# Optimization experiments

Hardware: AMD Instinct MI355X
Metric: run time of the kernel (lower is better)

## Reference

```python
import jax, jax.numpy as jnp
import numpy as np

D_MODEL = 1024
NUM_HEADS = 16
HEAD_SIZE = D_MODEL // NUM_HEADS
THETA = 10000.0
MAX_SEQ_LEN = 4096


def _rope_tables():
    # (max_seq_len, head_size//2) cos/sin tables, matching RotaryPositionalEmbedding
    k = jnp.arange(HEAD_SIZE // 2, dtype=jnp.float32)
    inv_freq = 1.0 / (THETA ** (2.0 * k / HEAD_SIZE))
    pos = jnp.arange(MAX_SEQ_LEN, dtype=jnp.float32)
    ang = pos[:, None] * inv_freq[None, :]
    return jnp.cos(ang), jnp.sin(ang)


def _apply_rope(x, cos, sin):
    # x: (b, h, s, d); cos/sin: (s, d//2) -> broadcast over (b, h)
    x1 = x[..., ::2]
    x2 = x[..., 1::2]
    out_even = x1 * cos - x2 * sin
    out_odd = x2 * cos + x1 * sin
    # re-interleave pairs back to (..., d)
    return jnp.stack([out_even, out_odd], axis=-1).reshape(x.shape)


def setup_inputs() -> dict:
    key = jax.random.key(0)
    k1, k2, k3 = jax.random.split(key, 3)
    b, s = 1, 4096
    std_qkv = np.sqrt(2.0 / (D_MODEL + 3 * D_MODEL))
    std_o = np.sqrt(2.0 / (D_MODEL + D_MODEL))
    return {
        "x": jax.random.normal(k1, (b, s, D_MODEL), dtype=jnp.float32),
        "token_positions": jnp.arange(s, dtype=jnp.int32),
        "W_qkv": jax.random.normal(k2, (3 * D_MODEL, D_MODEL), dtype=jnp.float32) * std_qkv,
        "W_o": jax.random.normal(k3, (D_MODEL, D_MODEL), dtype=jnp.float32) * std_o,
    }


def reference(x, token_positions, W_qkv, W_o):
    b, s, _ = x.shape
    qkv = jnp.einsum("bsd,ed->bse", x, W_qkv)  # (b, s, 3*d_model)
    q, k, v = jnp.split(qkv, 3, axis=-1)

    def to_heads(t):
        return t.reshape(b, s, NUM_HEADS, HEAD_SIZE).transpose(0, 2, 1, 3)  # (b, h, s, hs)

    q, k, v = to_heads(q), to_heads(k), to_heads(v)

    cos_tab, sin_tab = _rope_tables()
    cos = cos_tab[token_positions]  # (s, hs//2)
    sin = sin_tab[token_positions]
    q = _apply_rope(q, cos, sin)
    k = _apply_rope(k, cos, sin)

    scale = 1.0 / jnp.sqrt(jnp.asarray(HEAD_SIZE, dtype=x.dtype))
    scores = jnp.einsum("bhqd,bhkd->bhqk", q, k) * scale  # (b, h, s, s)
    causal = jnp.tril(jnp.ones((s, s), dtype=bool))
    scores = jnp.where(causal, scores, jnp.finfo(scores.dtype).min)
    attn = jax.nn.softmax(scores, axis=-1)
    out = jnp.einsum("bhqk,bhkd->bhqd", attn, v)  # (b, h, s, hs)
    out = out.transpose(0, 2, 1, 3).reshape(b, s, D_MODEL)
    return jnp.einsum("bsd,ed->bse", out, W_o)
```

## Files before the change

kernel.cpp:

```cpp
#include <hip/hip_runtime.h>
#include <stdint.h>

typedef unsigned short u16;
typedef __attribute__((ext_vector_type(8))) short bf16x8;
typedef __attribute__((ext_vector_type(4))) float f32x4;

#define LN_THETA 9.210340371976184f
#define SLEN 4096
#define DMODEL 1024

__device__ __forceinline__ u16 f2bf(float f) {
  union { float f; unsigned u; } v; v.f = f;
  unsigned u = v.u;
  return (u16)((u + 0x7FFFu + ((u >> 16) & 1u)) >> 16);
}
__device__ __forceinline__ u16 f2bf_trunc(float f) {
  union { float f; unsigned u; } v; v.f = f;
  return (u16)(v.u >> 16);
}

__device__ __forceinline__ f32x4 mfma16(bf16x8 a, bf16x8 b, f32x4 c) {
  return __builtin_amdgcn_mfma_f32_16x16x32_bf16(a, b, c, 0, 0, 0);
}

__device__ __forceinline__ void async16(const u16* g, u16* l) {
  __builtin_amdgcn_global_load_lds(
      (const __attribute__((address_space(1))) unsigned int*)g,
      (__attribute__((address_space(3))) unsigned int*)l, 16, 0, 0);
}

__global__ void rope_tab_kernel(const int* __restrict__ tokpos,
                                float2* __restrict__ tab) {
  int t = blockIdx.x * 256 + threadIdx.x;
  int s = t >> 5, i = t & 31;
  float inv = expf(-(float)(2 * i) * (LN_THETA / 64.0f));
  float ang = (float)tokpos[s] * inv;
  float sn, cs;
  sincosf(ang, &sn, &cs);
  tab[t] = make_float2(cs, sn);
}

__global__ void cvt_all_kernel(const float* __restrict__ x,
                               const float* __restrict__ wqkv,
                               const float* __restrict__ wo,
                               u16* __restrict__ xb, u16* __restrict__ wqkvb,
                               u16* __restrict__ wob) {
  int i = blockIdx.x * 256 + threadIdx.x;
  const float* src;
  u16* dst;
  if (i < (1 << 20)) {
    src = x; dst = xb;
  } else if (i < (1 << 20) + (3 << 18)) {
    i -= (1 << 20); src = wqkv; dst = wqkvb;
  } else {
    i -= (1 << 20) + (3 << 18); src = wo; dst = wob;
  }
  float4 v = ((const float4*)src)[i];
  ushort4 o;
  o.x = f2bf(v.x); o.y = f2bf(v.y); o.z = f2bf(v.z); o.w = f2bf(v.w);
  ((ushort4*)dst)[i] = o;
}

__global__ __launch_bounds__(256) void gemm_qkv_kernel(
    const u16* __restrict__ A, const u16* __restrict__ B,
    u16* __restrict__ qb, u16* __restrict__ kb,
    u16* __restrict__ vbT, const float2* __restrict__ cstab) {
  const int K = 1024;
  __shared__ __align__(16) u16 As[128][32];
  __shared__ __align__(16) u16 Bs[128][32];
  __shared__ __align__(16) u16 Ts[128][136];
  const int tid = threadIdx.x;
  const int wave = tid >> 6, lane = tid & 63;
  const int quad = lane >> 4, col = lane & 15;
  const int rowBase = blockIdx.x * 128;
  const int colBase = blockIdx.y * 128;
  const int wm = (wave >> 1) * 64, wn = (wave & 1) * 64;

  const int sRow = wave * 32 + (lane >> 2);
  const int sK = (lane & 3) * 8;
  const u16* gA = A + (size_t)(rowBase + sRow) * K + sK;
  const u16* gB = B + (size_t)(colBase + sRow) * K + sK;

  f32x4 acc[4][4];
#pragma unroll
  for (int i = 0; i < 4; ++i)
#pragma unroll
    for (int j = 0; j < 4; ++j)
      acc[i][j] = f32x4{0.f, 0.f, 0.f, 0.f};

  for (int kk = 0; kk < K; kk += 32) {
    __syncthreads();
    async16(gA + kk, &As[sRow][sK]);
    async16(gA + kk + 16 * K, &As[sRow + 16][sK]);
    async16(gB + kk, &Bs[sRow][sK]);
    async16(gB + kk + 16 * K, &Bs[sRow + 16][sK]);
    __syncthreads();
    bf16x8 af[4], bfr[4];
#pragma unroll
    for (int i = 0; i < 4; ++i)
      af[i] = *(const bf16x8*)&As[wm + i * 16 + col][quad * 8];
#pragma unroll
    for (int j = 0; j < 4; ++j)
      bfr[j] = *(const bf16x8*)&Bs[wn + j * 16 + col][quad * 8];
#pragma unroll
    for (int i = 0; i < 4; ++i)
#pragma unroll
      for (int j = 0; j < 4; ++j)
        acc[i][j] = mfma16(af[i], bfr[j], acc[i][j]);
  }

  const int sec = rowBase >> 10;

  if (sec < 2) {
#pragma unroll
    for (int j = 0; j < 4; ++j) {
      int sl = wn + j * 16 + col;
      int s = colBase + sl;
#pragma unroll
      for (int i = 0; i < 4; ++i) {
        int el = wm + i * 16 + quad * 4;
        int d = (rowBase + el) & 63;
        float v0 = acc[i][j][0], v1 = acc[i][j][1];
        float v2 = acc[i][j][2], v3 = acc[i][j][3];
        float2 cs0 = cstab[s * 32 + (d >> 1)];
        float2 cs1 = cstab[s * 32 + (d >> 1) + 1];
        ushort4 pk;
        pk.x = f2bf(v0 * cs0.x - v1 * cs0.y);
        pk.y = f2bf(v1 * cs0.x + v0 * cs0.y);
        pk.z = f2bf(v2 * cs1.x - v3 * cs1.y);
        pk.w = f2bf(v3 * cs1.x + v2 * cs1.y);
        *(ushort4*)&Ts[sl][el] = pk;
      }
    }
    __syncthreads();
    int sl = tid >> 1, hf = tid & 1;
    int hh = ((rowBase & 1023) >> 6) + hf;
    u16* dst = (sec == 0 ? qb : kb) + ((size_t)hh * SLEN + colBase + sl) * 64;
    const u16* srcp = &Ts[sl][hf * 64];
#pragma unroll
    for (int kq = 0; kq < 8; ++kq)
      ((int4*)dst)[kq] = ((const int4*)srcp)[kq];
  } else {
#pragma unroll
    for (int j = 0; j < 4; ++j) {
      int sl = wn + j * 16 + col;
#pragma unroll
      for (int i = 0; i < 4; ++i) {
        int el = wm + i * 16 + quad * 4;
#pragma unroll
        for (int r = 0; r < 4; ++r)
          Ts[el + r][sl] = f2bf(acc[i][j][r]);
      }
    }
    __syncthreads();
    int el = tid >> 1, sh = tid & 1;
    int e = rowBase - 2048 + el;
    int hh = e >> 6, d = e & 63;
    u16* dst = vbT + (size_t)(hh * 64 + d) * SLEN + colBase + sh * 64;
    const u16* srcp = &Ts[el][sh * 64];
#pragma unroll
    for (int kq = 0; kq < 8; ++kq)
      ((int4*)dst)[kq] = ((const int4*)srcp)[kq];
  }
}

__global__ __launch_bounds__(256) void gemm_out_kernel(
    const u16* __restrict__ A, const u16* __restrict__ B,
    float* __restrict__ outf) {
  const int K = 1024;
  __shared__ __align__(16) u16 As[128][32];
  __shared__ __align__(16) u16 Bs[64][32];
  const int tid = threadIdx.x;
  const int wave = tid >> 6, lane = tid & 63;
  const int quad = lane >> 4, col = lane & 15;
  const int rowBase = blockIdx.x * 128;
  const int colBase = blockIdx.y * 64;

  const int sRow = wave * 32 + (lane >> 2);
  const int bRow = wave * 16 + (lane >> 2);
  const int sK = (lane & 3) * 8;
  const u16* gA = A + (size_t)(rowBase + sRow) * K + sK;
  const u16* gB = B + (size_t)(colBase + bRow) * K + sK;

  f32x4 acc[2][4];
#pragma unroll
  for (int i = 0; i < 2; ++i)
#pragma unroll
    for (int j = 0; j < 4; ++j)
      acc[i][j] = f32x4{0.f, 0.f, 0.f, 0.f};

  for (int kk = 0; kk < K; kk += 32) {
    __syncthreads();
    async16(gA + kk, &As[sRow][sK]);
    async16(gA + kk + 16 * K, &As[sRow + 16][sK]);
    async16(gB + kk, &Bs[bRow][sK]);
    __syncthreads();
    bf16x8 af[2], bfr[4];
#pragma unroll
    for (int i = 0; i < 2; ++i)
      af[i] = *(const bf16x8*)&As[wave * 32 + i * 16 + col][quad * 8];
#pragma unroll
    for (int j = 0; j < 4; ++j)
      bfr[j] = *(const bf16x8*)&Bs[j * 16 + col][quad * 8];
#pragma unroll
    for (int i = 0; i < 2; ++i)
#pragma unroll
      for (int j = 0; j < 4; ++j)
        acc[i][j] = mfma16(af[i], bfr[j], acc[i][j]);
  }

#pragma unroll
  for (int i = 0; i < 2; ++i) {
    int r0 = rowBase + wave * 32 + i * 16 + quad * 4;
#pragma unroll
    for (int j = 0; j < 4; ++j) {
      int cc = colBase + j * 16 + col;
#pragma unroll
      for (int r = 0; r < 4; ++r)
        outf[(size_t)(r0 + r) * DMODEL + cc] = acc[i][j][r];
    }
  }
}

__global__ __launch_bounds__(128) void flash_kernel(
    const u16* __restrict__ qbuf, const u16* __restrict__ kbuf,
    const u16* __restrict__ vbT, u16* __restrict__ attn) {
  const int S = SLEN;
  const int h = blockIdx.x;
  const int tile = 63 - (int)blockIdx.y;
  const int wave = threadIdx.x >> 6, lane = threadIdx.x & 63;
  const int quad = lane >> 4, col = lane & 15;
  const u16* Q = qbuf + (size_t)h * S * 64;
  const u16* Kh = kbuf + (size_t)h * S * 64;
  const u16* Vt = vbT + (size_t)h * 64 * S;

  __shared__ __align__(16) u16 Ks[64][64];
  __shared__ __align__(16) u16 Vs[64][64];
  __shared__ __align__(16) u16 Pld[2][2][16][72];

  const int sr = lane >> 3;
  const int sw = ((lane & 7) ^ sr) * 8;
  const int dcol = (lane & 7) * 8;
  const int segA = ((quad ^ (col & 7)) * 8);
  const int segB = (((quad ^ 4) ^ (col & 7)) * 8);

  const int nch = tile + 1;
  const int qrow0 = tile * 64 + wave * 32;

  bf16x8 qf0[2], qf1[2];
#pragma unroll
  for (int i = 0; i < 2; ++i) {
    const u16* qp = &Q[(size_t)(qrow0 + i * 16 + col) * 64 + quad * 8];
    qf0[i] = *(const bf16x8*)qp;
    qf1[i] = *(const bf16x8*)(qp + 32);
  }

  f32x4 o[2][4];
#pragma unroll
  for (int i = 0; i < 2; ++i)
#pragma unroll
    for (int n = 0; n < 4; ++n) o[i][n] = f32x4{0.f, 0.f, 0.f, 0.f};
  float lrow[2][4] = {{0.f, 0.f, 0.f, 0.f}, {0.f, 0.f, 0.f, 0.f}};

  for (int c = 0; c < nch; ++c) {
    const int k0 = c * 64;
    __syncthreads();
    {
#pragma unroll
      for (int t = 0; t < 4; ++t) {
        int row = (t * 2 + wave) * 8 + sr;
        async16(Kh + (size_t)(k0 + row) * 64 + sw, &Ks[row][dcol]);
        async16(Vt + (size_t)row * S + k0 + sw, &Vs[row][dcol]);
      }
    }
    __syncthreads();

    bf16x8 kf0[4], kf1[4], vf0[4], vf1[4];
#pragma unroll
    for (int j = 0; j < 4; ++j) {
      kf0[j] = *(const bf16x8*)&Ks[16 * j + col][segA];
      kf1[j] = *(const bf16x8*)&Ks[16 * j + col][segB];
    }
#pragma unroll
    for (int n = 0; n < 4; ++n) {
      vf0[n] = *(const bf16x8*)&Vs[16 * n + col][segA];
      vf1[n] = *(const bf16x8*)&Vs[16 * n + col][segB];
    }
    const bool lastc = (c == nch - 1);
#pragma unroll
    for (int i = 0; i < 2; ++i) {
      f32x4 s[4];
#pragma unroll
      for (int j = 0; j < 4; ++j)
        s[j] = mfma16(qf1[i], kf1[j],
                      mfma16(qf0[i], kf0[j], f32x4{0.f, 0.f, 0.f, 0.f}));
      float p[4][4];
#pragma unroll
      for (int r = 0; r < 4; ++r) {
        const int qrel = wave * 32 + i * 16 + quad * 4 + r;
#pragma unroll
        for (int j = 0; j < 4; ++j) {
          float e = __expf(s[j][r] * 0.125f);
          if (lastc && (16 * j + col > qrel)) e = 0.f;
          p[j][r] = e;
        }
        lrow[i][r] += (p[0][r] + p[1][r]) + (p[2][r] + p[3][r]);
      }
#pragma unroll
      for (int j = 0; j < 4; ++j)
#pragma unroll
        for (int r = 0; r < 4; ++r)
          Pld[wave][i][quad * 4 + r][16 * j + col] = f2bf_trunc(p[j][r]);
      bf16x8 pa0 = *(const bf16x8*)&Pld[wave][i][col][quad * 8];
      bf16x8 pa1 = *(const bf16x8*)&Pld[wave][i][col][quad * 8 + 32];
#pragma unroll
      for (int n = 0; n < 4; ++n)
        o[i][n] = mfma16(pa1, vf1[n], mfma16(pa0, vf0[n], o[i][n]));
    }
  }

#pragma unroll
  for (int i = 0; i < 2; ++i) {
#pragma unroll
    for (int m = 1; m <= 8; m <<= 1)
#pragma unroll
      for (int r = 0; r < 4; ++r) lrow[i][r] += __shfl_xor(lrow[i][r], m);
#pragma unroll
    for (int r = 0; r < 4; ++r) {
      float inv = 1.0f / lrow[i][r];
      int row = qrow0 + i * 16 + quad * 4 + r;
      u16* dst = &attn[(size_t)row * DMODEL + h * 64 + col];
#pragma unroll
      for (int n = 0; n < 4; ++n) dst[16 * n] = f2bf(o[i][n][r] * inv);
    }
  }
}

extern "C" void kernel_launch(void* const* d_in, const int* in_sizes, int n_in,
                              void* d_out, int out_size, void* d_ws,
                              size_t ws_size, hipStream_t stream) {
  const float* x = (const float*)d_in[0];
  const int* tokpos = (const int*)d_in[1];
  const float* wqkv = (const float*)d_in[2];
  const float* wo = (const float*)d_in[3];
  float* out = (float*)d_out;

  char* ws = (char*)d_ws;
  u16* xb    = (u16*)(ws);
  u16* wqkvb = (u16*)(ws + ((size_t)8 << 20));
  u16* wob   = (u16*)(ws + ((size_t)14 << 20));
  u16* qb    = (u16*)(ws + ((size_t)16 << 20));
  u16* kb    = (u16*)(ws + ((size_t)24 << 20));
  u16* vbT   = (u16*)(ws + ((size_t)32 << 20));
  u16* attn  = (u16*)(ws + ((size_t)40 << 20));
  float2* cstab = (float2*)(ws + ((size_t)48 << 20));

  rope_tab_kernel<<<dim3(512), dim3(256), 0, stream>>>(tokpos, cstab);
  cvt_all_kernel<<<dim3(8192), dim3(256), 0, stream>>>(x, wqkv, wo, xb, wqkvb,
                                                       wob);
  gemm_qkv_kernel<<<dim3(24, 32), dim3(256), 0, stream>>>(
      wqkvb, xb, qb, kb, vbT, cstab);
  flash_kernel<<<dim3(16, 64), dim3(128), 0, stream>>>(qb, kb, vbT, attn);
  gemm_out_kernel<<<dim3(32, 16), dim3(256), 0, stream>>>(attn, wob, out);
}
```

Before: 246.4 us.

## Split long causal query tiles across two blocks and merge with a reduction kernel

```diff
diff --git a/kernel.cpp b/kernel.cpp
--- a/kernel.cpp
+++ b/kernel.cpp
@@ -17,6 +17,10 @@
 __device__ __forceinline__ u16 f2bf_trunc(float f) {
   union { float f; unsigned u; } v; v.f = f;
   return (u16)(v.u >> 16);
+}
+__device__ __forceinline__ float bf2f(u16 b) {
+  union { unsigned u; float f; } v; v.u = ((unsigned)b) << 16;
+  return v.f;
 }
 
 __device__ __forceinline__ f32x4 mfma16(bf16x8 a, bf16x8 b, f32x4 c) {
@@ -224,10 +228,21 @@
 
 __global__ __launch_bounds__(128) void flash_kernel(
     const u16* __restrict__ qbuf, const u16* __restrict__ kbuf,
-    const u16* __restrict__ vbT, u16* __restrict__ attn) {
+    const u16* __restrict__ vbT, u16* __restrict__ po,
+    float* __restrict__ pl) {
   const int S = SLEN;
   const int h = blockIdx.x;
-  const int tile = 63 - (int)blockIdx.y;
+  const int y = blockIdx.y;
+  int tile, c0, c1;
+  if (y < 32) {
+    tile = 32 + y; c0 = 0; c1 = 31;
+  } else {
+    int k = (y - 32) >> 1;
+    if ((y - 32) & 1) { tile = 31 - k; c0 = 0; c1 = tile; }
+    else { tile = 63 - k; c0 = 32; c1 = tile; }
+  }
+  const int id = (tile < 32) ? tile : (32 + 2 * (tile - 32) + (c0 ? 1 : 0));
+
   const int wave = threadIdx.x >> 6, lane = threadIdx.x & 63;
   const int quad = lane >> 4, col = lane & 15;
   const u16* Q = qbuf + (size_t)h * S * 64;
@@ -244,7 +259,6 @@
   const int segA = ((quad ^ (col & 7)) * 8);
   const int segB = (((quad ^ 4) ^ (col & 7)) * 8);
 
-  const int nch = tile + 1;
   const int qrow0 = tile * 64 + wave * 32;
 
   bf16x8 qf0[2], qf1[2];
@@ -262,7 +276,7 @@
     for (int n = 0; n < 4; ++n) o[i][n] = f32x4{0.f, 0.f, 0.f, 0.f};
   float lrow[2][4] = {{0.f, 0.f, 0.f, 0.f}, {0.f, 0.f, 0.f, 0.f}};
 
-  for (int c = 0; c < nch; ++c) {
+  for (int c = c0; c <= c1; ++c) {
     const int k0 = c * 64;
     __syncthreads();
     {
@@ -286,7 +300,7 @@
       vf0[n] = *(const bf16x8*)&Vs[16 * n + col][segA];
       vf1[n] = *(const bf16x8*)&Vs[16 * n + col][segB];
     }
-    const bool lastc = (c == nch - 1);
+    const bool lastc = (c == tile);
 #pragma unroll
     for (int i = 0; i < 2; ++i) {
       f32x4 s[4];
@@ -319,6 +333,8 @@
     }
   }
 
+  u16* pob = po + (((size_t)h * 96 + id) * 64) * 64;
+  float* plb = pl + ((size_t)h * 96 + id) * 64;
 #pragma unroll
   for (int i = 0; i < 2; ++i) {
 #pragma unroll
@@ -327,13 +343,49 @@
       for (int r = 0; r < 4; ++r) lrow[i][r] += __shfl_xor(lrow[i][r], m);
 #pragma unroll
     for (int r = 0; r < 4; ++r) {
-      float inv = 1.0f / lrow[i][r];
-      int row = qrow0 + i * 16 + quad * 4 + r;
-      u16* dst = &attn[(size_t)row * DMODEL + h * 64 + col];
-#pragma unroll
-      for (int n = 0; n < 4; ++n) dst[16 * n] = f2bf(o[i][n][r] * inv);
-    }
-  }
+      int rowl = wave * 32 + i * 16 + quad * 4 + r;
+      u16* dst = pob + (size_t)rowl * 64 + col;
+#pragma unroll
+      for (int n = 0; n < 4; ++n) dst[16 * n] = f2bf(o[i][n][r]);
+      if (col == 0) plb[rowl] = lrow[i][r];
+    }
+  }
+}
+
+__global__ __launch_bounds__(256) void reduce_kernel(
+    const u16* __restrict__ po, const float* __restrict__ pl,
+    u16* __restrict__ attn) {
+  const int h = blockIdx.x, tile = blockIdx.y;
+  const int tid = threadIdx.x;
+  const int row = tid >> 2, dg = (tid & 3) * 16;
+  int id0, ns;
+  if (tile < 32) { id0 = tile; ns = 1; }
+  else { id0 = 32 + 2 * (tile - 32); ns = 2; }
+
+  float acc[16];
+#pragma unroll
+  for (int q = 0; q < 16; ++q) acc[q] = 0.f;
+  float l = 0.f;
+  for (int s = 0; s < ns; ++s) {
+    const size_t base = ((size_t)h * 96 + id0 + s) * 64;
+    const u16* p = po + (base + row) * 64 + dg;
+    l += pl[base + row];
+#pragma unroll
+    for (int q = 0; q < 16; ++q) acc[q] += bf2f(p[q]);
+  }
+  float inv = 1.0f / l;
+  u16* dst = attn + (size_t)(tile * 64 + row) * DMODEL + h * 64 + dg;
+  ushort4 o0, o1, o2, o3;
+  o0.x = f2bf(acc[0] * inv);  o0.y = f2bf(acc[1] * inv);
+  o0.z = f2bf(acc[2] * inv);  o0.w = f2bf(acc[3] * inv);
+  o1.x = f2bf(acc[4] * inv);  o1.y = f2bf(acc[5] * inv);
+  o1.z = f2bf(acc[6] * inv);  o1.w = f2bf(acc[7] * inv);
+  o2.x = f2bf(acc[8] * inv);  o2.y = f2bf(acc[9] * inv);
+  o2.z = f2bf(acc[10] * inv); o2.w = f2bf(acc[11] * inv);
+  o3.x = f2bf(acc[12] * inv); o3.y = f2bf(acc[13] * inv);
+  o3.z = f2bf(acc[14] * inv); o3.w = f2bf(acc[15] * inv);
+  ((ushort4*)dst)[0] = o0; ((ushort4*)dst)[1] = o1;
+  ((ushort4*)dst)[2] = o2; ((ushort4*)dst)[3] = o3;
 }
 
 extern "C" void kernel_launch(void* const* d_in, const int* in_sizes, int n_in,
@@ -354,12 +406,15 @@
   u16* vbT   = (u16*)(ws + ((size_t)32 << 20));
   u16* attn  = (u16*)(ws + ((size_t)40 << 20));
   float2* cstab = (float2*)(ws + ((size_t)48 << 20));
+  u16* po    = (u16*)(ws);
+  float* pl  = (float*)(ws + ((size_t)13 << 20));
 
   rope_tab_kernel<<<dim3(512), dim3(256), 0, stream>>>(tokpos, cstab);
   cvt_all_kernel<<<dim3(8192), dim3(256), 0, stream>>>(x, wqkv, wo, xb, wqkvb,
                                                        wob);
   gemm_qkv_kernel<<<dim3(24, 32), dim3(256), 0, stream>>>(
       wqkvb, xb, qb, kb, vbT, cstab);
-  flash_kernel<<<dim3(16, 64), dim3(128), 0, stream>>>(qb, kb, vbT, attn);
+  flash_kernel<<<dim3(16, 96), dim3(128), 0, stream>>>(qb, kb, vbT, po, pl);
+  reduce_kernel<<<dim3(16, 64), dim3(256), 0, stream>>>(po, pl, attn);
   gemm_out_kernel<<<dim3(32, 16), dim3(256), 0, stream>>>(attn, wob, out);
 }
```

Result: faster. 232.5 us (-5.6%).
